# Optimization experiments

Measured on AMD Instinct MI355X. Metric: run time of the kernel, lower is better.

Reference implementation:

```python
import jax, jax.numpy as jnp
import numpy as np

N = 8192   # nodes per graph
F = 128    # input feature dim
H = 512    # GAT hidden dim
D = 256    # GAT output dim (== match_size, required by matching broadcast)
MS = 256   # match_size
E = 131072 # edges per graph (one direction)
EPS = 1e-8 # torch cosine_similarity eps


def _xavier(k, shape):
    lim = (6.0 / (shape[0] + shape[-1])) ** 0.5
    return jax.random.uniform(k, shape, jnp.float32, -lim, lim)


def setup_inputs() -> dict:
    key = jax.random.key(0)
    ks = jax.random.split(key, 24)
    return {
        "x_s": jax.random.normal(ks[0], (N, F), jnp.float32),
        "x_t": jax.random.normal(ks[1], (N, F), jnp.float32),
        "edge_index_s": jax.random.randint(ks[2], (2, E), 0, N),
        "edge_index_t": jax.random.randint(ks[3], (2, E), 0, N),
        "label": jax.random.randint(ks[4], (1,), 0, 2),
        # GAT params (2 single-head layers)
        "W_g1": _xavier(ks[5], (F, H)),
        "a1_src": _xavier(ks[6], (H, 1))[:, 0],
        "a1_dst": _xavier(ks[7], (H, 1))[:, 0],
        "W_g2": _xavier(ks[8], (H, D)),
        "a2_src": _xavier(ks[9], (D, 1))[:, 0],
        "a2_dst": _xavier(ks[10], (D, 1))[:, 0],
        # readout_rep
        "W_read": _xavier(ks[11], (D, D)),
        # matching
        "W_match": _xavier(ks[12], (D, MS)),
        # MLP
        "mlp_w1": _xavier(ks[13], (MS * 8, MS * 2)), "mlp_b1": jnp.zeros((MS * 2,), jnp.float32),
        "mlp_w2": _xavier(ks[14], (MS * 2, MS)),     "mlp_b2": jnp.zeros((MS,), jnp.float32),
        "mlp_w3": _xavier(ks[15], (MS, MS // 2)),    "mlp_b3": jnp.zeros((MS // 2,), jnp.float32),
        "mlp_w4": _xavier(ks[16], (MS // 2, 1)),     "mlp_b4": jnp.zeros((1,), jnp.float32),
    }


def _gat_layer(h_in, src, dst, W, a_s, a_d, n):
    h = h_in @ W                                           # [n, d_out]
    logits = (h[src] * a_s).sum(-1) + (h[dst] * a_d).sum(-1)
    e = jax.nn.leaky_relu(logits, 0.2)
    m = jax.ops.segment_max(e, dst, num_segments=n)
    ex = jnp.exp(e - m[dst])
    den = jax.ops.segment_sum(ex, dst, num_segments=n)
    alpha = ex / (den[dst] + 1e-16)
    return jax.ops.segment_sum(alpha[:, None] * h[src], dst, num_segments=n)


def _gat(x, edge_index, W1, a1s, a1d, W2, a2s, a2d):
    n = x.shape[0]
    sl = jnp.arange(n)
    # symmetrize undirected edge list + add self loops (PyG GATConv convention)
    src = jnp.concatenate([edge_index[0], edge_index[1], sl])
    dst = jnp.concatenate([edge_index[1], edge_index[0], sl])
    h = jax.nn.elu(_gat_layer(x, src, dst, W1, a1s, a1d, n))
    return _gat_layer(h, src, dst, W2, a2s, a2d, n)


def _readout(h, W):
    g = jnp.tanh(jnp.mean(h, 0) @ W)                       # [d]
    s = jax.nn.sigmoid(h @ g)                              # [n]
    return (s[:, None] * h).sum(0, keepdims=True)          # [1, d]


def _match(h1, h2, Wm):
    # cosine over feature dim of (h * W) without materializing [N, D, MS]:
    # dot[n,m] = sum_d h1[n,d]*W[d,m]*h2[n,d]*W[d,m] = ((h1*h2) @ W^2)[n,m]
    W2 = Wm * Wm
    dot = (h1 * h2) @ W2
    n1 = jnp.sqrt((h1 * h1) @ W2)
    n2 = jnp.sqrt((h2 * h2) @ W2)
    return dot / jnp.maximum(n1 * n2, EPS)


def _mutual(h1, h2):
    n1 = jnp.linalg.norm(h1, axis=-1)
    n2 = jnp.linalg.norm(h2, axis=-1)
    cos = (h1 @ h2.T) / jnp.maximum(n1[:, None] * n2[None, :], EPS)  # [N, M]
    coe = cos / cos.sum(0)                                 # column-normalize
    return coe @ h2


def _mlp(z, w1, b1, w2, b2, w3, b3, w4, b4):
    z = jax.nn.relu(z @ w1 + b1)
    z = jax.nn.relu(z @ w2 + b2)
    z = jax.nn.relu(z @ w3 + b3)
    return jax.nn.sigmoid(z @ w4 + b4)


def _forward(x_s, x_t, edge_index_s, edge_index_t, label,
             W_g1, a1_src, a1_dst, W_g2, a2_src, a2_dst,
             W_read, W_match,
             mlp_w1, mlp_b1, mlp_w2, mlp_b2, mlp_w3, mlp_b3, mlp_w4, mlp_b4):
    f1 = (x_s - jnp.mean(x_s)) / jnp.std(x_s, ddof=1)
    f2 = (x_t - jnp.mean(x_t)) / jnp.std(x_t, ddof=1)

    h1 = _gat(f1, edge_index_s, W_g1, a1_src, a1_dst, W_g2, a2_src, a2_dst)
    h2 = _gat(f2, edge_index_t, W_g1, a1_src, a1_dst, W_g2, a2_src, a2_dst)

    h1g = _readout(h1, W_read)
    h2g = _readout(h2, W_read)

    h1m = _mutual(h1, h2)
    h2m = _mutual(h2, h1)
    h1mg = _readout(h1m, W_read)
    h2mg = _readout(h2m, W_read)

    miu1 = _match(h1, h1m, W_match); miu2 = _match(h2, h2m, W_match)
    miu1g = _readout(miu1, W_read);  miu2g = _readout(miu2, W_read)
    phi1 = _match(h1, h1mg, W_match); phi2 = _match(h2, h2mg, W_match)
    phi1g = _readout(phi1, W_read);   phi2g = _readout(phi2, W_read)
    psi1 = _match(h1g, h1m, W_match); psi2 = _match(h2g, h2m, W_match)
    psi1g = _readout(psi1, W_read);   psi2g = _readout(psi2, W_read)
    om1 = _match(h1g, h1mg, W_match); om2 = _match(h2g, h2mg, W_match)

    z1 = jnp.concatenate([miu1g, phi1g, psi1g, om1], axis=1).T  # [4*MS, 1]
    z2 = jnp.concatenate([miu2g, phi2g, psi2g, om2], axis=1).T
    z = jnp.concatenate([z1, z2], axis=0).T                     # [1, 8*MS]
    z = _mlp(z, mlp_w1, mlp_b1, mlp_w2, mlp_b2, mlp_w3, mlp_b3, mlp_w4, mlp_b4)
    return z


def reference(x_s, x_t, edge_index_s, edge_index_t, label,
              W_g1, a1_src, a1_dst, W_g2, a2_src, a2_dst,
              W_read, W_match,
              mlp_w1, mlp_b1, mlp_w2, mlp_b2, mlp_w3, mlp_b3, mlp_w4, mlp_b4):
    z = _forward(x_s, x_t, edge_index_s, edge_index_t, label,
                 W_g1, a1_src, a1_dst, W_g2, a2_src, a2_dst, W_read, W_match,
                 mlp_w1, mlp_b1, mlp_w2, mlp_b2, mlp_w3, mlp_b3, mlp_w4, mlp_b4)
    label_exp = jnp.exp(-label.astype(jnp.float32))
    return z, label, label_exp
```

## Files before the change

kernel.cpp:

```cpp
#include <hip/hip_runtime.h>
#include <hip/hip_bf16.h>
#include <math.h>
#include <stddef.h>

#define NN 8192
#define FF 128
#define HH 512
#define DDIM 256
#define EE 131072
#define ET (2*EE + NN)
#define FEPS 1e-8f

typedef float f32x4 __attribute__((ext_vector_type(4)));
typedef __bf16 bf16x8 __attribute__((ext_vector_type(8)));
typedef unsigned short u16;

static __device__ __forceinline__ u16 f2bf(float f) {
  union { float f; unsigned u; } v; v.f = f;
  return (u16)((v.u + 0x7fffu + ((v.u >> 16) & 1u)) >> 16);
}
static __device__ __forceinline__ float bf2f(u16 h) {
  union { unsigned u; float f; } v; v.u = ((unsigned)h) << 16;
  return v.f;
}
static __device__ __forceinline__ f32x4 mfma16(bf16x8 a, bf16x8 b, f32x4 c) {
  return __builtin_amdgcn_mfma_f32_16x16x32_bf16(a, b, c, 0, 0, 0);
}

struct PLB { const u16* p[6]; int slot[6]; };
struct MM {
  const u16* A1[6]; const u16* A2[6]; const u16* B[6];
  const u16* R1[6]; const u16* R2[6]; const float* Y[6]; u16* o[6];
};

__global__ void k_reduce2(const float* __restrict__ xa, const float* __restrict__ xb,
                          int n, double* __restrict__ out) {
  const float* x = blockIdx.y ? xb : xa;
  double* o = out + 2 * blockIdx.y;
  __shared__ double s1[256], s2[256];
  double a = 0.0, b = 0.0;
  for (int i = blockIdx.x * blockDim.x + threadIdx.x; i < n; i += gridDim.x * blockDim.x) {
    double v = (double)x[i];
    a += v; b += v * v;
  }
  s1[threadIdx.x] = a; s2[threadIdx.x] = b;
  __syncthreads();
  for (int w = 128; w > 0; w >>= 1) {
    if (threadIdx.x < w) { s1[threadIdx.x] += s1[threadIdx.x + w]; s2[threadIdx.x] += s2[threadIdx.x + w]; }
    __syncthreads();
  }
  if (threadIdx.x == 0) { atomicAdd(&o[0], s1[0]); atomicAdd(&o[1], s2[0]); }
}

__global__ void k_normalize2(const float* __restrict__ xa, const float* __restrict__ xb,
                             u16* __restrict__ ya, u16* __restrict__ yb, int n,
                             const double* __restrict__ s) {
  const float* x = blockIdx.y ? xb : xa;
  u16* y = blockIdx.y ? yb : ya;
  const double* sp = s + 2 * blockIdx.y;
  double mean = sp[0] / (double)n;
  double var = (sp[1] - (double)n * mean * mean) / (double)(n - 1);
  float mu = (float)mean;
  float inv = (float)(1.0 / sqrt(var));
  for (int i = blockIdx.x * blockDim.x + threadIdx.x; i < n; i += gridDim.x * blockDim.x)
    y[i] = f2bf((x[i] - mu) * inv);
}

__global__ void k_hist(const int* __restrict__ ei, int* __restrict__ deg) {
  int t = blockIdx.x * blockDim.x + threadIdx.x;
  if (t >= ET) return;
  int dst = (t < EE) ? ei[EE + t] : ((t < 2*EE) ? ei[t - EE] : (t - 2*EE));
  atomicAdd(&deg[dst], 1);
}

__global__ void k_scan(const int* __restrict__ deg, int* __restrict__ offs, int* __restrict__ cursor) {
  __shared__ int ts[256];
  int tid = threadIdx.x;
  int loc[32];
  int s = 0;
  #pragma unroll
  for (int i = 0; i < 32; ++i) { loc[i] = s; s += deg[tid * 32 + i]; }
  ts[tid] = s;
  __syncthreads();
  for (int off = 1; off < 256; off <<= 1) {
    int v = (tid >= off) ? ts[tid - off] : 0;
    __syncthreads();
    ts[tid] += v;
    __syncthreads();
  }
  int pre = ts[tid] - s;
  #pragma unroll
  for (int i = 0; i < 32; ++i) {
    int o = pre + loc[i];
    offs[tid * 32 + i] = o;
    cursor[tid * 32 + i] = o;
  }
  if (tid == 255) offs[NN] = ts[255];
}

__global__ void k_scatter(const int* __restrict__ ei, int* __restrict__ cursor, int* __restrict__ srcs) {
  int t = blockIdx.x * blockDim.x + threadIdx.x;
  if (t >= ET) return;
  int src = (t < 2*EE) ? ei[t] : (t - 2*EE);
  int dst = (t < EE) ? ei[EE + t] : ((t < 2*EE) ? ei[t - EE] : (t - 2*EE));
  int pos = atomicAdd(&cursor[dst], 1);
  srcs[pos] = src;
}

__global__ __launch_bounds__(256) void k_tr_bf16(const float* __restrict__ src, u16* __restrict__ dst,
                                                 int R, int C, int sq) {
  __shared__ float T[32][33];
  int tx = threadIdx.x & 31, ty = threadIdx.x >> 5;
  int r0 = blockIdx.y * 32, c0 = blockIdx.x * 32;
  #pragma unroll
  for (int p = 0; p < 4; ++p)
    T[ty + 8 * p][tx] = src[(size_t)(r0 + ty + 8 * p) * C + c0 + tx];
  __syncthreads();
  #pragma unroll
  for (int p = 0; p < 4; ++p) {
    float v = T[tx][ty + 8 * p];
    if (sq) v *= v;
    dst[(size_t)(c0 + ty + 8 * p) * R + r0 + tx] = f2bf(v);
  }
}

__global__ __launch_bounds__(256) void k_tr2w(const float* __restrict__ hA, const float* __restrict__ scA,
                                              u16* __restrict__ tA, u16* __restrict__ wA,
                                              const float* __restrict__ hB, const float* __restrict__ scB,
                                              u16* __restrict__ tB, u16* __restrict__ wB) {
  __shared__ float T[32][33];
  __shared__ float W[32][33];
  const float* src = blockIdx.z ? hB : hA;
  const float* sc  = blockIdx.z ? scB : scA;
  u16* dt = blockIdx.z ? tB : tA;
  u16* dw = blockIdx.z ? wB : wA;
  int tx = threadIdx.x & 31, ty = threadIdx.x >> 5;
  int r0 = blockIdx.y * 32, c0 = blockIdx.x * 32;
  #pragma unroll
  for (int p = 0; p < 4; ++p) {
    int j = r0 + ty + 8 * p;
    float v = src[(size_t)j * DDIM + c0 + tx];
    T[ty + 8 * p][tx] = v;
    W[ty + 8 * p][tx] = v * sc[j];
  }
  __syncthreads();
  #pragma unroll
  for (int p = 0; p < 4; ++p) {
    size_t o = (size_t)(c0 + ty + 8 * p) * NN + r0 + tx;
    dt[o] = f2bf(T[tx][ty + 8 * p]);
    dw[o] = f2bf(W[tx][ty + 8 * p]);
  }
}

__global__ __launch_bounds__(256) void k_gemm_bf(const u16* __restrict__ A, const u16* __restrict__ Bt,
                                                 u16* __restrict__ Cb, int K, int N,
                                                 const float* __restrict__ as_, const float* __restrict__ ad_,
                                                 float* __restrict__ hs, float* __restrict__ hd) {
  int w = threadIdx.x >> 6, l = threadIdx.x & 63, r15 = l & 15, g = l >> 4;
  int i0 = blockIdx.y * 64 + w * 16;
  int n0 = blockIdx.x * 128;
  f32x4 zero = {0.f, 0.f, 0.f, 0.f};
  f32x4 acc[8];
  #pragma unroll
  for (int n = 0; n < 8; ++n) acc[n] = zero;
  int kcN = K >> 5;
  const u16* arow = A + (size_t)(i0 + r15) * K + g * 8;
  for (int kc = 0; kc < kcN; ++kc) {
    bf16x8 a = *reinterpret_cast<const bf16x8*>(arow + kc * 32);
    #pragma unroll
    for (int n = 0; n < 8; ++n) {
      bf16x8 b = *reinterpret_cast<const bf16x8*>(Bt + (size_t)(n0 + n * 16 + r15) * K + kc * 32 + g * 8);
      acc[n] = mfma16(a, b, acc[n]);
    }
  }
  int io = i0 + g * 4;
  #pragma unroll
  for (int n = 0; n < 8; ++n) {
    int c = n0 + n * 16 + r15;
    #pragma unroll
    for (int q = 0; q < 4; ++q)
      Cb[(size_t)(io + q) * N + c] = f2bf(acc[n][q]);
  }
  if (as_) {
    float hsum[4] = {0.f, 0.f, 0.f, 0.f}, dsum[4] = {0.f, 0.f, 0.f, 0.f};
    #pragma unroll
    for (int n = 0; n < 8; ++n) {
      int c = n0 + n * 16 + r15;
      float av = as_[c], dv = ad_[c];
      #pragma unroll
      for (int q = 0; q < 4; ++q) { hsum[q] += acc[n][q] * av; dsum[q] += acc[n][q] * dv; }
    }
    #pragma unroll
    for (int q = 0; q < 4; ++q) {
      #pragma unroll
      for (int o = 1; o < 16; o <<= 1) { hsum[q] += __shfl_xor(hsum[q], o); dsum[q] += __shfl_xor(dsum[q], o); }
    }
    if (r15 == 0) {
      #pragma unroll
      for (int q = 0; q < 4; ++q) {
        atomicAdd(&hs[io + q], hsum[q]);
        atomicAdd(&hd[io + q], dsum[q]);
      }
    }
  }
}

__global__ void k_alpha(const int* __restrict__ offs, const int* __restrict__ srcs,
                        const float* __restrict__ hs, const float* __restrict__ hd,
                        float* __restrict__ alpha) {
  int wid = (blockIdx.x * blockDim.x + threadIdx.x) >> 6;
  int lane = threadIdx.x & 63;
  if (wid >= NN) return;
  int b = offs[wid], e = offs[wid + 1];
  float hdn = hd[wid];
  float m = -3.4e38f;
  for (int p = b + lane; p < e; p += 64) {
    float v = hs[srcs[p]] + hdn;
    v = v > 0.f ? v : 0.2f * v;
    alpha[p] = v;
    m = fmaxf(m, v);
  }
  #pragma unroll
  for (int o = 32; o > 0; o >>= 1) m = fmaxf(m, __shfl_xor(m, o));
  float den = 0.f;
  for (int p = b + lane; p < e; p += 64) {
    float ex = expf(alpha[p] - m);
    alpha[p] = ex;
    den += ex;
  }
  #pragma unroll
  for (int o = 32; o > 0; o >>= 1) den += __shfl_xor(den, o);
  float sc = 1.f / (den + 1e-16f);
  for (int p = b + lane; p < e; p += 64) alpha[p] *= sc;
}

__global__ __launch_bounds__(256) void k_agg3(const int* __restrict__ offs, const int* __restrict__ srcs,
                                              const float* __restrict__ alpha, const u16* __restrict__ Hb,
                                              float* __restrict__ outF, u16* __restrict__ outB,
                                              int D, int elu) {
  int wv = threadIdx.x >> 6, lane = threadIdx.x & 63;
  int n = blockIdx.x * 4 + wv;
  int b = offs[n], e = offs[n + 1];
  if (D == 512) {
    float acc[8];
    #pragma unroll
    for (int j = 0; j < 8; ++j) acc[j] = 0.f;
    const u16* base = Hb + lane * 8;
    for (int p = b; p < e; ++p) {
      float a = alpha[p];
      uint4 v = *reinterpret_cast<const uint4*>(base + (size_t)srcs[p] * 512);
      acc[0] += a * bf2f((u16)(v.x & 0xffff)); acc[1] += a * bf2f((u16)(v.x >> 16));
      acc[2] += a * bf2f((u16)(v.y & 0xffff)); acc[3] += a * bf2f((u16)(v.y >> 16));
      acc[4] += a * bf2f((u16)(v.z & 0xffff)); acc[5] += a * bf2f((u16)(v.z >> 16));
      acc[6] += a * bf2f((u16)(v.w & 0xffff)); acc[7] += a * bf2f((u16)(v.w >> 16));
    }
    ushort4 o0, o1;
    #pragma unroll
    for (int j = 0; j < 8; ++j)
      if (elu) acc[j] = acc[j] > 0.f ? acc[j] : (expf(acc[j]) - 1.f);
    o0.x = f2bf(acc[0]); o0.y = f2bf(acc[1]); o0.z = f2bf(acc[2]); o0.w = f2bf(acc[3]);
    o1.x = f2bf(acc[4]); o1.y = f2bf(acc[5]); o1.z = f2bf(acc[6]); o1.w = f2bf(acc[7]);
    u16* ob = outB + (size_t)n * 512 + lane * 8;
    *reinterpret_cast<ushort4*>(ob) = o0;
    *reinterpret_cast<ushort4*>(ob + 4) = o1;
  } else {
    float acc[4];
    #pragma unroll
    for (int j = 0; j < 4; ++j) acc[j] = 0.f;
    const u16* base = Hb + lane * 4;
    for (int p = b; p < e; ++p) {
      float a = alpha[p];
      uint2 v = *reinterpret_cast<const uint2*>(base + (size_t)srcs[p] * 256);
      acc[0] += a * bf2f((u16)(v.x & 0xffff)); acc[1] += a * bf2f((u16)(v.x >> 16));
      acc[2] += a * bf2f((u16)(v.y & 0xffff)); acc[3] += a * bf2f((u16)(v.y >> 16));
    }
    #pragma unroll
    for (int j = 0; j < 4; ++j)
      if (elu) acc[j] = acc[j] > 0.f ? acc[j] : (expf(acc[j]) - 1.f);
    if (outF) {
      float4 of = {acc[0], acc[1], acc[2], acc[3]};
      *reinterpret_cast<float4*>(outF + (size_t)n * 256 + lane * 4) = of;
    }
    ushort4 ob;
    ob.x = f2bf(acc[0]); ob.y = f2bf(acc[1]); ob.z = f2bf(acc[2]); ob.w = f2bf(acc[3]);
    *reinterpret_cast<ushort4*>(outB + (size_t)n * 256 + lane * 4) = ob;
  }
}

__global__ void k_rninv2(const float* __restrict__ h1, const float* __restrict__ h2,
                         float* __restrict__ o1, float* __restrict__ o2) {
  const float* h = blockIdx.y ? h2 : h1;
  float* o = blockIdx.y ? o2 : o1;
  int wid = (blockIdx.x * blockDim.x + threadIdx.x) >> 6;
  int lane = threadIdx.x & 63;
  if (wid >= NN) return;
  float4 v = *reinterpret_cast<const float4*>(h + (size_t)wid * DDIM + lane * 4);
  float a = v.x * v.x + v.y * v.y + v.z * v.z + v.w * v.w;
  #pragma unroll
  for (int o2_ = 32; o2_ > 0; o2_ >>= 1) a += __shfl_xor(a, o2_);
  if (!lane) o[wid] = 1.f / sqrtf(a);
}

__global__ void k_wsum(const float* __restrict__ h1, const float* __restrict__ h2,
                       const float* __restrict__ n1inv, const float* __restrict__ n2inv,
                       float* __restrict__ ut) {
  const float* h = blockIdx.y ? h2 : h1;
  const float* wv = blockIdx.y ? n2inv : n1inv;
  float* o = ut + 256 * blockIdx.y;
  int d = threadIdx.x;
  int r0 = blockIdx.x * 128;
  float acc = 0.f;
  for (int r = 0; r < 128; ++r) acc += wv[r0 + r] * h[(size_t)(r0 + r) * 256 + d];
  atomicAdd(&o[d], acc);
}

__global__ void k_rs(const float* __restrict__ h1, const float* __restrict__ h2,
                     const float* __restrict__ n1inv, const float* __restrict__ n2inv,
                     const float* __restrict__ ut, float* __restrict__ R, float* __restrict__ S) {
  const float* h  = blockIdx.y ? h2 : h1;
  const float* ni = blockIdx.y ? n2inv : n1inv;
  const float* gv = blockIdx.y ? ut : ut + 256;
  float* o = blockIdx.y ? S : R;
  int wid = (blockIdx.x * blockDim.x + threadIdx.x) >> 6;
  int lane = threadIdx.x & 63;
  if (wid >= NN) return;
  float4 v = *reinterpret_cast<const float4*>(h + (size_t)wid * 256 + lane * 4);
  float4 g4 = *reinterpret_cast<const float4*>(gv + lane * 4);
  float a = v.x * g4.x + v.y * g4.y + v.z * g4.z + v.w * g4.w;
  #pragma unroll
  for (int o2_ = 32; o2_ > 0; o2_ >>= 1) a += __shfl_xor(a, o2_);
  if (!lane) o[wid] = ni[wid] * a;
}

__global__ void k_scj(const float* __restrict__ S, const float* __restrict__ R,
                      const float* __restrict__ n1inv, const float* __restrict__ n2inv,
                      float* __restrict__ scj1, float* __restrict__ scj2) {
  int j = blockIdx.x * blockDim.x + threadIdx.x;
  if (j >= NN) return;
  scj1[j] = n2inv[j] / S[j];
  scj2[j] = n1inv[j] / R[j];
}

__global__ __launch_bounds__(256) void k_gemm_M(const u16* __restrict__ A1, const u16* __restrict__ B1,
                                                const u16* __restrict__ A2, const u16* __restrict__ B2,
                                                float* __restrict__ Mf) {
  int mat = blockIdx.z & 1, kch = blockIdx.z >> 1;
  const u16* A = mat ? A2 : A1;
  const u16* Bt = mat ? B2 : B1;
  float* C = Mf + mat * 65536;
  int w = threadIdx.x >> 6, l = threadIdx.x & 63, r15 = l & 15, g = l >> 4;
  int i0 = blockIdx.y * 64 + w * 16;
  int n0 = blockIdx.x * 128;
  f32x4 zero = {0.f, 0.f, 0.f, 0.f};
  f32x4 acc[8];
  #pragma unroll
  for (int n = 0; n < 8; ++n) acc[n] = zero;
  const u16* arow = A + (size_t)(i0 + r15) * NN + g * 8;
  for (int kc = kch * 16; kc < kch * 16 + 16; ++kc) {
    bf16x8 a = *reinterpret_cast<const bf16x8*>(arow + kc * 32);
    #pragma unroll
    for (int n = 0; n < 8; ++n) {
      bf16x8 b = *reinterpret_cast<const bf16x8*>(Bt + (size_t)(n0 + n * 16 + r15) * NN + kc * 32 + g * 8);
      acc[n] = mfma16(a, b, acc[n]);
    }
  }
  int io = i0 + g * 4;
  #pragma unroll
  for (int n = 0; n < 8; ++n) {
    int c = n0 + n * 16 + r15;
    #pragma unroll
    for (int q = 0; q < 4; ++q)
      atomicAdd(&C[(size_t)(io + q) * 256 + c], acc[n][q]);
  }
}

__global__ void k_m2bf(const float* __restrict__ Mf, u16* __restrict__ Mb) {
  size_t o = (size_t)blockIdx.y * 65536 + blockIdx.x * 256 + threadIdx.x;
  Mb[o] = f2bf(Mf[o]);
}

__global__ __launch_bounds__(256) void k_gemm_hm(const u16* __restrict__ A1, const u16* __restrict__ M1,
                                                 const float* __restrict__ s1, u16* __restrict__ O1,
                                                 const u16* __restrict__ A2, const u16* __restrict__ M2,
                                                 const float* __restrict__ s2, u16* __restrict__ O2) {
  int z = blockIdx.z;
  const u16* A = z ? A2 : A1;
  const u16* Bt = z ? M2 : M1;
  const float* sc = z ? s2 : s1;
  u16* O = z ? O2 : O1;
  int w = threadIdx.x >> 6, l = threadIdx.x & 63, r15 = l & 15, g = l >> 4;
  int i0 = blockIdx.y * 64 + w * 16;
  int n0 = blockIdx.x * 128;
  f32x4 zero = {0.f, 0.f, 0.f, 0.f};
  f32x4 acc[8];
  #pragma unroll
  for (int n = 0; n < 8; ++n) acc[n] = zero;
  const u16* arow = A + (size_t)(i0 + r15) * 256 + g * 8;
  #pragma unroll
  for (int kc = 0; kc < 8; ++kc) {
    bf16x8 a = *reinterpret_cast<const bf16x8*>(arow + kc * 32);
    #pragma unroll
    for (int n = 0; n < 8; ++n) {
      bf16x8 b = *reinterpret_cast<const bf16x8*>(Bt + (size_t)(n0 + n * 16 + r15) * 256 + kc * 32 + g * 8);
      acc[n] = mfma16(a, b, acc[n]);
    }
  }
  int io = i0 + g * 4;
  float s4[4];
  #pragma unroll
  for (int q = 0; q < 4; ++q) s4[q] = sc[io + q];
  #pragma unroll
  for (int n = 0; n < 8; ++n) {
    int c = n0 + n * 16 + r15;
    #pragma unroll
    for (int q = 0; q < 4; ++q)
      O[(size_t)(io + q) * 256 + c] = f2bf(acc[n][q] * s4[q]);
  }
}

__global__ __launch_bounds__(256) void k_matchA(const u16* __restrict__ A0, const u16* __restrict__ A1,
                                                const u16* __restrict__ A2_, const u16* __restrict__ A3,
                                                const u16* __restrict__ W2t,
                                                u16* __restrict__ r0, u16* __restrict__ r1,
                                                u16* __restrict__ r2, u16* __restrict__ r3) {
  int z = blockIdx.z;
  const u16* A = z == 0 ? A0 : z == 1 ? A1 : z == 2 ? A2_ : A3;
  u16* outR = z == 0 ? r0 : z == 1 ? r1 : z == 2 ? r2 : r3;
  int w = threadIdx.x >> 6, l = threadIdx.x & 63, r15 = l & 15, g = l >> 4;
  int i0 = blockIdx.y * 64 + w * 16;
  int n0 = blockIdx.x * 128;
  f32x4 zero = {0.f, 0.f, 0.f, 0.f};
  f32x4 acc[8];
  #pragma unroll
  for (int n = 0; n < 8; ++n) acc[n] = zero;
  const u16* arow = A + (size_t)(i0 + r15) * 256 + g * 8;
  #pragma unroll
  for (int kc = 0; kc < 8; ++kc) {
    uint4 xv = *reinterpret_cast<const uint4*>(arow + kc * 32);
    bf16x8 fp;
    float t;
    t = bf2f((u16)(xv.x & 0xffff)); fp[0] = (__bf16)(t * t);
    t = bf2f((u16)(xv.x >> 16));    fp[1] = (__bf16)(t * t);
    t = bf2f((u16)(xv.y & 0xffff)); fp[2] = (__bf16)(t * t);
    t = bf2f((u16)(xv.y >> 16));    fp[3] = (__bf16)(t * t);
    t = bf2f((u16)(xv.z & 0xffff)); fp[4] = (__bf16)(t * t);
    t = bf2f((u16)(xv.z >> 16));    fp[5] = (__bf16)(t * t);
    t = bf2f((u16)(xv.w & 0xffff)); fp[6] = (__bf16)(t * t);
    t = bf2f((u16)(xv.w >> 16));    fp[7] = (__bf16)(t * t);
    #pragma unroll
    for (int n = 0; n < 8; ++n) {
      bf16x8 b = *reinterpret_cast<const bf16x8*>(W2t + (size_t)(n0 + n * 16 + r15) * 256 + kc * 32 + g * 8);
      acc[n] = mfma16(fp, b, acc[n]);
    }
  }
  int io = i0 + g * 4;
  #pragma unroll
  for (int n = 0; n < 8; ++n) {
    int c = n0 + n * 16 + r15;
    #pragma unroll
    for (int q = 0; q < 4; ++q)
      outR[(size_t)(io + q) * 256 + c] = f2bf(rsqrtf(fmaxf(acc[n][q], 1e-30f)));
  }
}

__global__ void k_w2d(const u16* __restrict__ W2t, const float* __restrict__ ogs,
                      u16* __restrict__ W2d, float* __restrict__ yn) {
  __shared__ float red[256];
  int n = blockIdx.x, z = blockIdx.y, k = threadIdx.x;
  int map = (z == 0) ? 512 : (z == 1) ? 0 : (z == 2) ? 768 : 256;
  float y = ogs[map + k];
  float wv = bf2f(W2t[n * 256 + k]);
  W2d[z * 65536 + n * 256 + k] = f2bf(wv * y);
  red[k] = wv * y * y;
  __syncthreads();
  for (int s = 128; s > 0; s >>= 1) {
    if (k < s) red[k] += red[k + s];
    __syncthreads();
  }
  if (!k) yn[z * 256 + n] = rsqrtf(fmaxf(red[0], 1e-30f));
}

__global__ __launch_bounds__(256) void k_matchB(MM M) {
  int z = blockIdx.z;
  const u16* A1 = M.A1[z];
  const u16* A2 = M.A2[z];
  const u16* Bt = M.B[z];
  const u16* R1 = M.R1[z];
  const u16* R2 = M.R2[z];
  const float* Y = M.Y[z];
  u16* outb = M.o[z];
  int w = threadIdx.x >> 6, l = threadIdx.x & 63, r15 = l & 15, g = l >> 4;
  int i0 = blockIdx.y * 64 + w * 16;
  int n0 = blockIdx.x * 128;
  f32x4 zero = {0.f, 0.f, 0.f, 0.f};
  f32x4 acc[8];
  #pragma unroll
  for (int n = 0; n < 8; ++n) acc[n] = zero;
  size_t abase = (size_t)(i0 + r15) * 256 + g * 8;
  #pragma unroll
  for (int kc = 0; kc < 8; ++kc) {
    bf16x8 fa;
    uint4 a = *reinterpret_cast<const uint4*>(A1 + abase + kc * 32);
    if (A2) {
      uint4 b2 = *reinterpret_cast<const uint4*>(A2 + abase + kc * 32);
      fa[0] = (__bf16)(bf2f((u16)(a.x & 0xffff)) * bf2f((u16)(b2.x & 0xffff)));
      fa[1] = (__bf16)(bf2f((u16)(a.x >> 16))    * bf2f((u16)(b2.x >> 16)));
      fa[2] = (__bf16)(bf2f((u16)(a.y & 0xffff)) * bf2f((u16)(b2.y & 0xffff)));
      fa[3] = (__bf16)(bf2f((u16)(a.y >> 16))    * bf2f((u16)(b2.y >> 16)));
      fa[4] = (__bf16)(bf2f((u16)(a.z & 0xffff)) * bf2f((u16)(b2.z & 0xffff)));
      fa[5] = (__bf16)(bf2f((u16)(a.z >> 16))    * bf2f((u16)(b2.z >> 16)));
      fa[6] = (__bf16)(bf2f((u16)(a.w & 0xffff)) * bf2f((u16)(b2.w & 0xffff)));
      fa[7] = (__bf16)(bf2f((u16)(a.w >> 16))    * bf2f((u16)(b2.w >> 16)));
    } else {
      fa = *reinterpret_cast<const bf16x8*>(&a);
    }
    #pragma unroll
    for (int n = 0; n < 8; ++n) {
      bf16x8 b = *reinterpret_cast<const bf16x8*>(Bt + (size_t)(n0 + n * 16 + r15) * 256 + kc * 32 + g * 8);
      acc[n] = mfma16(fa, b, acc[n]);
    }
  }
  int io = i0 + g * 4;
  #pragma unroll
  for (int n = 0; n < 8; ++n) {
    int c = n0 + n * 16 + r15;
    float yc = Y ? Y[c] : 1.f;
    #pragma unroll
    for (int q = 0; q < 4; ++q) {
      float sc = yc;
      size_t idx = (size_t)(io + q) * 256 + c;
      if (R1) sc *= bf2f(R1[idx]);
      if (R2) sc *= bf2f(R2[idx]);
      outb[idx] = f2bf(acc[n][q] * sc);
    }
  }
}

__global__ void k_match_g(const float* __restrict__ X1, const float* __restrict__ Y1,
                          const float* __restrict__ X2, const float* __restrict__ Y2,
                          const float* __restrict__ W2, float* __restrict__ v) {
  __shared__ float u[256], p[256], q[256];
  const float* X = blockIdx.x ? X2 : X1;
  const float* Y = blockIdx.x ? Y2 : Y1;
  float* o = v + (blockIdx.x ? 1792 : 768);
  int t = threadIdx.x;
  float xv = X[t], yv = Y[t];
  u[t] = xv * yv; p[t] = xv * xv; q[t] = yv * yv;
  __syncthreads();
  float a = 0.f, b = 0.f, c = 0.f;
  #pragma unroll 4
  for (int d = 0; d < 256; ++d) {
    float wv = W2[(size_t)d * DDIM + t];
    a += u[d] * wv; b += p[d] * wv; c += q[d] * wv;
  }
  o[t] = a / fmaxf(sqrtf(b) * sqrtf(c), FEPS);
}

__global__ void k_w2(const float* __restrict__ Wm, float* __restrict__ W2, int n) {
  int i = blockIdx.x * blockDim.x + threadIdx.x;
  if (i < n) { float v = Wm[i]; W2[i] = v * v; }
}

__global__ void k_bmu_b(PLB L, float* __restrict__ mu) {
  const u16* h = L.p[blockIdx.y];
  int d = threadIdx.x;
  int r0 = blockIdx.x * 128;
  float acc = 0.f;
  for (int r = 0; r < 128; ++r) acc += bf2f(h[(size_t)(r0 + r) * 256 + d]);
  atomicAdd(&mu[blockIdx.y * 256 + d], acc);
}

__global__ void k_bgv(const float* __restrict__ mu, const float* __restrict__ Wr,
                      float* __restrict__ g) {
  __shared__ float ls[256];
  int m = blockIdx.x, t = threadIdx.x;
  ls[t] = mu[m * 256 + t] * (1.f / (float)NN);
  __syncthreads();
  float acc = 0.f;
  #pragma unroll 4
  for (int d = 0; d < 256; ++d) acc += ls[d] * Wr[(size_t)d * 256 + t];
  g[m * 256 + t] = tanhf(acc);
}

__global__ __launch_bounds__(256) void k_bsc_b(PLB L, const float* __restrict__ g,
                                               float* __restrict__ v) {
  __shared__ __align__(16) float gs[256];
  __shared__ float sarr[32];
  int m = blockIdx.y;
  const u16* h = L.p[m];
  int t = threadIdx.x, w = t >> 6, l = t & 63;
  gs[t] = g[m * 256 + t];
  __syncthreads();
  int r0 = blockIdx.x * 32;
  float4 gv4 = reinterpret_cast<const float4*>(gs)[l];
  for (int rr = w * 8; rr < w * 8 + 8; ++rr) {
    ushort4 hv = *reinterpret_cast<const ushort4*>(h + (size_t)(r0 + rr) * 256 + l * 4);
    float dot = bf2f(hv.x) * gv4.x + bf2f(hv.y) * gv4.y + bf2f(hv.z) * gv4.z + bf2f(hv.w) * gv4.w;
    #pragma unroll
    for (int o = 32; o > 0; o >>= 1) dot += __shfl_xor(dot, o);
    if (!l) sarr[rr] = 1.f / (1.f + expf(-dot));
  }
  __syncthreads();
  float acc = 0.f;
  for (int rr = 0; rr < 32; ++rr) acc += sarr[rr] * bf2f(h[(size_t)(r0 + rr) * 256 + t]);
  atomicAdd(&v[L.slot[m] + t], acc);
}

__global__ void k_binit(const float* __restrict__ b1, const float* __restrict__ b2,
                        const float* __restrict__ b3, float* __restrict__ l1,
                        float* __restrict__ l2, float* __restrict__ l3) {
  int t = blockIdx.x * 256 + threadIdx.x;
  if (t < 512) l1[t] = b1[t];
  if (t < 256) l2[t] = b2[t];
  if (t < 128) l3[t] = b3[t];
}

__global__ void k_gemv(const float* __restrict__ vin, const float* __restrict__ w,
                       float* __restrict__ out, int K, int M, int Kc, int relu_in) {
  int m = blockIdx.x * 256 + threadIdx.x;
  if (m >= M) return;
  int k0 = blockIdx.y * Kc;
  float acc = 0.f;
  #pragma unroll 4
  for (int k = k0; k < k0 + Kc; ++k) {
    float x = vin[k];
    if (relu_in) x = fmaxf(x, 0.f);
    acc += x * w[(size_t)k * M + m];
  }
  atomicAdd(&out[m], acc);
}

__global__ void k_final(const float* __restrict__ l3, const float* __restrict__ w4,
                        const float* __restrict__ b4, const int* __restrict__ label,
                        float* __restrict__ out) {
  __shared__ float ls[128];
  int t = threadIdx.x;
  ls[t] = fmaxf(l3[t], 0.f) * w4[t];
  __syncthreads();
  for (int w = 64; w > 0; w >>= 1) { if (t < w) ls[t] += ls[t + w]; __syncthreads(); }
  if (t == 0) {
    float z = 1.f / (1.f + expf(-(ls[0] + b4[0])));
    out[0] = z;
    float lb = (float)label[0];
    out[1] = lb;
    out[2] = expf(-lb);
  }
}

extern "C" void kernel_launch(void* const* d_in, const int* in_sizes, int n_in,
                              void* d_out, int out_size, void* d_ws, size_t ws_size,
                              hipStream_t stream) {
  (void)in_sizes; (void)n_in; (void)out_size;
  const float* x_s   = (const float*)d_in[0];
  const float* x_t   = (const float*)d_in[1];
  const int*   ei_s  = (const int*)d_in[2];
  const int*   ei_t  = (const int*)d_in[3];
  const int*   label = (const int*)d_in[4];
  const float* W_g1  = (const float*)d_in[5];
  const float* a1s   = (const float*)d_in[6];
  const float* a1d   = (const float*)d_in[7];
  const float* W_g2  = (const float*)d_in[8];
  const float* a2s   = (const float*)d_in[9];
  const float* a2d   = (const float*)d_in[10];
  const float* W_read  = (const float*)d_in[11];
  const float* W_match = (const float*)d_in[12];
  const float* w1 = (const float*)d_in[13]; const float* b1 = (const float*)d_in[14];
  const float* w2 = (const float*)d_in[15]; const float* b2 = (const float*)d_in[16];
  const float* w3 = (const float*)d_in[17]; const float* b3 = (const float*)d_in[18];
  const float* w4 = (const float*)d_in[19]; const float* b4 = (const float*)d_in[20];
  float* out = (float*)d_out;

  char* base = (char*)d_ws;
  size_t off = 0;
  auto alloc = [&](size_t bytes) -> void* {
    void* pp = base + off;
    off = (off + bytes + 255) & ~(size_t)255;
    return pp;
  };
  double* dsum = (double*)alloc(4 * sizeof(double));
  u16*   hb_bf= (u16*)alloc((size_t)NN * HH * 2);
  u16*   aggb = (u16*)alloc((size_t)NN * HH * 2);
  float* h1   = (float*)alloc((size_t)NN * DDIM * 4);
  float* h2   = (float*)alloc((size_t)NN * DDIM * 4);
  u16*   f1b  = (u16*)alloc((size_t)NN * FF * 2);
  u16*   f2b  = (u16*)alloc((size_t)NN * FF * 2);
  u16*   h1b  = (u16*)alloc((size_t)NN * DDIM * 2);
  u16*   h2b  = (u16*)alloc((size_t)NN * DDIM * 2);
  u16*   h1mb = (u16*)alloc((size_t)NN * DDIM * 2);
  u16*   h2mb = (u16*)alloc((size_t)NN * DDIM * 2);
  u16*   h1t  = (u16*)alloc((size_t)NN * DDIM * 2);
  u16*   h2t  = (u16*)alloc((size_t)NN * DDIM * 2);
  u16*   wh1t = (u16*)alloc((size_t)NN * DDIM * 2);
  u16*   wh2t = (u16*)alloc((size_t)NN * DDIM * 2);
  u16*   mb0  = (u16*)alloc((size_t)NN * DDIM * 2);
  u16*   mb1  = (u16*)alloc((size_t)NN * DDIM * 2);
  u16*   mb2  = (u16*)alloc((size_t)NN * DDIM * 2);
  u16*   mb3  = (u16*)alloc((size_t)NN * DDIM * 2);
  u16*   mb4  = (u16*)alloc((size_t)NN * DDIM * 2);
  u16*   mb5  = (u16*)alloc((size_t)NN * DDIM * 2);
  u16*   rP1  = (u16*)alloc((size_t)NN * DDIM * 2);
  u16*   rQ1  = (u16*)alloc((size_t)NN * DDIM * 2);
  u16*   rP2  = (u16*)alloc((size_t)NN * DDIM * 2);
  u16*   rQ2  = (u16*)alloc((size_t)NN * DDIM * 2);
  float* alpha= (float*)alloc((size_t)ET * 4);
  int*   srcs = (int*)alloc((size_t)ET * 4);
  int*   deg  = (int*)alloc(NN * 4);
  int*   curs = (int*)alloc(NN * 4);
  int*   offs = (int*)alloc((NN + 1) * 4);
  float* n1inv= (float*)alloc(NN * 4);
  float* n2inv= (float*)alloc(NN * 4);
  float* Rr   = (float*)alloc(NN * 4);
  float* Ss   = (float*)alloc(NN * 4);
  float* scj1 = (float*)alloc(NN * 4);
  float* scj2 = (float*)alloc(NN * 4);
  float* hsb  = (float*)alloc(NN * 4);
  float* hdb  = (float*)alloc(NN * 4);
  float* W2   = (float*)alloc((size_t)DDIM * DDIM * 4);
  u16*   Wg1t = (u16*)alloc((size_t)HH * FF * 2);
  u16*   Wg2t = (u16*)alloc((size_t)DDIM * HH * 2);
  u16*   W2t  = (u16*)alloc((size_t)DDIM * DDIM * 2);
  u16*   W2dB = (u16*)alloc(4 * 65536 * 2);
  float* ynB  = (float*)alloc(4 * 256 * 4);
  u16*   Mb   = (u16*)alloc(2 * 65536 * 2);
  float* mug1 = (float*)alloc(4 * 256 * 4);
  float* ogs  = (float*)alloc(4 * 256 * 4);
  float* mug2 = (float*)alloc(6 * 256 * 4);
  float* v    = (float*)alloc(2048 * 4);
  float* ut   = (float*)alloc(512 * 4);
  float* Mf   = (float*)alloc(2 * 65536 * 4);
  float* g1   = (float*)alloc(4 * 256 * 4);
  float* g2   = (float*)alloc(6 * 256 * 4);
  float* l1o  = (float*)alloc(512 * 4);
  float* l2o  = (float*)alloc(256 * 4);
  float* l3o  = (float*)alloc(128 * 4);
  if (off > ws_size) return;

  float* h1g  = ogs + 0;
  float* h2g  = ogs + 256;
  float* h1mg = ogs + 512;
  float* h2mg = ogs + 768;
  const size_t zr_bytes = (4 * 256 + 4 * 256 + 6 * 256 + 2048 + 512 + 2 * 65536) * 4;

  hipMemsetAsync(dsum, 0, 4 * sizeof(double), stream);
  k_reduce2<<<dim3(1024, 2), 256, 0, stream>>>(x_s, x_t, NN * FF, dsum);
  k_normalize2<<<dim3(1024, 2), 256, 0, stream>>>(x_s, x_t, f1b, f2b, NN * FF, dsum);

  k_tr_bf16<<<dim3(HH / 32, FF / 32), 256, 0, stream>>>(W_g1, Wg1t, FF, HH, 0);
  k_tr_bf16<<<dim3(DDIM / 32, HH / 32), 256, 0, stream>>>(W_g2, Wg2t, HH, DDIM, 0);
  k_tr_bf16<<<dim3(DDIM / 32, DDIM / 32), 256, 0, stream>>>(W_match, W2t, DDIM, DDIM, 1);
  k_w2<<<dim3((DDIM * DDIM + 255) / 256), 256, 0, stream>>>(W_match, W2, DDIM * DDIM);

  auto run_gat = [&](const u16* finb, const int* ei, float* hout, u16* houtb) {
    hipMemsetAsync(deg, 0, NN * 4, stream);
    k_hist<<<dim3((ET + 255) / 256), 256, 0, stream>>>(ei, deg);
    k_scan<<<1, 256, 0, stream>>>(deg, offs, curs);
    k_scatter<<<dim3((ET + 255) / 256), 256, 0, stream>>>(ei, curs, srcs);
    hipMemsetAsync(hsb, 0, 2 * NN * 4, stream);
    k_gemm_bf<<<dim3(HH / 128, NN / 64), 256, 0, stream>>>(finb, Wg1t, hb_bf, FF, HH, a1s, a1d, hsb, hdb);
    k_alpha<<<dim3(NN / 4), 256, 0, stream>>>(offs, srcs, hsb, hdb, alpha);
    k_agg3<<<dim3(NN / 4), 256, 0, stream>>>(offs, srcs, alpha, hb_bf, nullptr, aggb, HH, 1);
    hipMemsetAsync(hsb, 0, 2 * NN * 4, stream);
    k_gemm_bf<<<dim3(DDIM / 128, NN / 64), 256, 0, stream>>>(aggb, Wg2t, hb_bf, HH, DDIM, a2s, a2d, hsb, hdb);
    k_alpha<<<dim3(NN / 4), 256, 0, stream>>>(offs, srcs, hsb, hdb, alpha);
    k_agg3<<<dim3(NN / 4), 256, 0, stream>>>(offs, srcs, alpha, hb_bf, hout, houtb, DDIM, 0);
  };
  run_gat(f1b, ei_s, h1, h1b);
  run_gat(f2b, ei_t, h2, h2b);

  k_rninv2<<<dim3(NN / 4, 2), 256, 0, stream>>>(h1, h2, n1inv, n2inv);
  hipMemsetAsync(mug1, 0, zr_bytes, stream);
  k_wsum<<<dim3(64, 2), 256, 0, stream>>>(h1, h2, n1inv, n2inv, ut);
  k_rs<<<dim3(NN / 4, 2), 256, 0, stream>>>(h1, h2, n1inv, n2inv, ut, Rr, Ss);
  k_scj<<<dim3(NN / 256), 256, 0, stream>>>(Ss, Rr, n1inv, n2inv, scj1, scj2);
  k_tr2w<<<dim3(DDIM / 32, NN / 32, 2), 256, 0, stream>>>(h2, scj1, h2t, wh2t, h1, scj2, h1t, wh1t);
  k_gemm_M<<<dim3(2, 4, 32), 256, 0, stream>>>(wh2t, h2t, wh1t, h1t, Mf);
  k_m2bf<<<dim3(256, 2), 256, 0, stream>>>(Mf, Mb);
  k_gemm_hm<<<dim3(2, 128, 2), 256, 0, stream>>>(h1b, Mb, n1inv, h1mb,
                                                 h2b, Mb + 65536, n2inv, h2mb);

  k_matchA<<<dim3(2, 128, 4), 256, 0, stream>>>(h1b, h1mb, h2b, h2mb, W2t, rP1, rQ1, rP2, rQ2);

  PLB g1l;
  g1l.p[0] = h1b;  g1l.slot[0] = 0;
  g1l.p[1] = h2b;  g1l.slot[1] = 256;
  g1l.p[2] = h1mb; g1l.slot[2] = 512;
  g1l.p[3] = h2mb; g1l.slot[3] = 768;
  k_bmu_b<<<dim3(64, 4), 256, 0, stream>>>(g1l, mug1);
  k_bgv<<<dim3(4), 256, 0, stream>>>(mug1, W_read, g1);
  k_bsc_b<<<dim3(256, 4), 256, 0, stream>>>(g1l, g1, ogs);

  k_w2d<<<dim3(256, 4), 256, 0, stream>>>(W2t, ogs, W2dB, ynB);
  MM m;
  m.A1[0] = h1b;  m.A2[0] = h1mb;    m.B[0] = W2t;            m.R1[0] = rP1; m.R2[0] = rQ1;    m.Y[0] = nullptr;   m.o[0] = mb0;
  m.A1[1] = h1b;  m.A2[1] = nullptr; m.B[1] = W2dB;           m.R1[1] = rP1; m.R2[1] = nullptr; m.Y[1] = ynB;       m.o[1] = mb1;
  m.A1[2] = h1mb; m.A2[2] = nullptr; m.B[2] = W2dB + 65536;   m.R1[2] = rQ1; m.R2[2] = nullptr; m.Y[2] = ynB + 256; m.o[2] = mb2;
  m.A1[3] = h2b;  m.A2[3] = h2mb;    m.B[3] = W2t;            m.R1[3] = rP2; m.R2[3] = rQ2;    m.Y[3] = nullptr;   m.o[3] = mb3;
  m.A1[4] = h2b;  m.A2[4] = nullptr; m.B[4] = W2dB + 2*65536; m.R1[4] = rP2; m.R2[4] = nullptr; m.Y[4] = ynB + 512; m.o[4] = mb4;
  m.A1[5] = h2mb; m.A2[5] = nullptr; m.B[5] = W2dB + 3*65536; m.R1[5] = rQ2; m.R2[5] = nullptr; m.Y[5] = ynB + 768; m.o[5] = mb5;
  k_matchB<<<dim3(2, NN / 64, 6), 256, 0, stream>>>(m);
  k_match_g<<<dim3(2), 256, 0, stream>>>(h1g, h1mg, h2g, h2mg, W2, v);

  PLB g2l;
  g2l.p[0] = mb0; g2l.slot[0] = 0;
  g2l.p[1] = mb1; g2l.slot[1] = 256;
  g2l.p[2] = mb2; g2l.slot[2] = 512;
  g2l.p[3] = mb3; g2l.slot[3] = 1024;
  g2l.p[4] = mb4; g2l.slot[4] = 1280;
  g2l.p[5] = mb5; g2l.slot[5] = 1536;
  k_bmu_b<<<dim3(64, 6), 256, 0, stream>>>(g2l, mug2);
  k_bgv<<<dim3(6), 256, 0, stream>>>(mug2, W_read, g2);
  k_bsc_b<<<dim3(256, 6), 256, 0, stream>>>(g2l, g2, v);

  k_binit<<<dim3(2), 256, 0, stream>>>(b1, b2, b3, l1o, l2o, l3o);
  k_gemv<<<dim3(2, 16), 256, 0, stream>>>(v, w1, l1o, 2048, 512, 128, 0);
  k_gemv<<<dim3(1, 8), 256, 0, stream>>>(l1o, w2, l2o, 512, 256, 64, 1);
  k_gemv<<<dim3(1, 8), 256, 0, stream>>>(l2o, w3, l3o, 256, 128, 32, 1);
  k_final<<<1, 128, 0, stream>>>(l3o, w4, b4, label, out);
}
```

Baseline: 746.4 us.

## Fuse match norm GEMMs and matching GEMMs into one kernel per graph

Merges k_matchA, which computed rsqrt norm matrices and stored them, with k_matchB, which reread them to scale the six matching outputs, into a single kernel. Each block now loads h and hm once and runs five MFMA accumulations (P, Q, U, phi, psi) over a 64-column tile, applying the rsqrt scaling in registers. This removes four NN×256 intermediate buffers, their writes and reads, and one launch. In exchange it holds more accumulator registers per thread, which may lower occupancy.

```diff
diff --git a/kernel.cpp b/kernel.cpp
--- a/kernel.cpp
+++ b/kernel.cpp
@@ -28,10 +28,6 @@
 }
 
 struct PLB { const u16* p[6]; int slot[6]; };
-struct MM {
-  const u16* A1[6]; const u16* A2[6]; const u16* B[6];
-  const u16* R1[6]; const u16* R2[6]; const float* Y[6]; u16* o[6];
-};
 
 __global__ void k_reduce2(const float* __restrict__ xa, const float* __restrict__ xb,
                           int n, double* __restrict__ out) {
@@ -418,51 +414,6 @@
   }
 }
 
-__global__ __launch_bounds__(256) void k_matchA(const u16* __restrict__ A0, const u16* __restrict__ A1,
-                                                const u16* __restrict__ A2_, const u16* __restrict__ A3,
-                                                const u16* __restrict__ W2t,
-                                                u16* __restrict__ r0, u16* __restrict__ r1,
-                                                u16* __restrict__ r2, u16* __restrict__ r3) {
-  int z = blockIdx.z;
-  const u16* A = z == 0 ? A0 : z == 1 ? A1 : z == 2 ? A2_ : A3;
-  u16* outR = z == 0 ? r0 : z == 1 ? r1 : z == 2 ? r2 : r3;
-  int w = threadIdx.x >> 6, l = threadIdx.x & 63, r15 = l & 15, g = l >> 4;
-  int i0 = blockIdx.y * 64 + w * 16;
-  int n0 = blockIdx.x * 128;
-  f32x4 zero = {0.f, 0.f, 0.f, 0.f};
-  f32x4 acc[8];
-  #pragma unroll
-  for (int n = 0; n < 8; ++n) acc[n] = zero;
-  const u16* arow = A + (size_t)(i0 + r15) * 256 + g * 8;
-  #pragma unroll
-  for (int kc = 0; kc < 8; ++kc) {
-    uint4 xv = *reinterpret_cast<const uint4*>(arow + kc * 32);
-    bf16x8 fp;
-    float t;
-    t = bf2f((u16)(xv.x & 0xffff)); fp[0] = (__bf16)(t * t);
-    t = bf2f((u16)(xv.x >> 16));    fp[1] = (__bf16)(t * t);
-    t = bf2f((u16)(xv.y & 0xffff)); fp[2] = (__bf16)(t * t);
-    t = bf2f((u16)(xv.y >> 16));    fp[3] = (__bf16)(t * t);
-    t = bf2f((u16)(xv.z & 0xffff)); fp[4] = (__bf16)(t * t);
-    t = bf2f((u16)(xv.z >> 16));    fp[5] = (__bf16)(t * t);
-    t = bf2f((u16)(xv.w & 0xffff)); fp[6] = (__bf16)(t * t);
-    t = bf2f((u16)(xv.w >> 16));    fp[7] = (__bf16)(t * t);
-    #pragma unroll
-    for (int n = 0; n < 8; ++n) {
-      bf16x8 b = *reinterpret_cast<const bf16x8*>(W2t + (size_t)(n0 + n * 16 + r15) * 256 + kc * 32 + g * 8);
-      acc[n] = mfma16(fp, b, acc[n]);
-    }
-  }
-  int io = i0 + g * 4;
-  #pragma unroll
-  for (int n = 0; n < 8; ++n) {
-    int c = n0 + n * 16 + r15;
-    #pragma unroll
-    for (int q = 0; q < 4; ++q)
-      outR[(size_t)(io + q) * 256 + c] = f2bf(rsqrtf(fmaxf(acc[n][q], 1e-30f)));
-  }
-}
-
 __global__ void k_w2d(const u16* __restrict__ W2t, const float* __restrict__ ogs,
                       u16* __restrict__ W2d, float* __restrict__ yn) {
   __shared__ float red[256];
@@ -480,58 +431,80 @@
   if (!k) yn[z * 256 + n] = rsqrtf(fmaxf(red[0], 1e-30f));
 }
 
-__global__ __launch_bounds__(256) void k_matchB(MM M) {
+__global__ __launch_bounds__(256) void k_match5(
+    const u16* __restrict__ h1b, const u16* __restrict__ h1mb,
+    const u16* __restrict__ h2b, const u16* __restrict__ h2mb,
+    const u16* __restrict__ W2t, const u16* __restrict__ W2dB, const float* __restrict__ ynB,
+    u16* __restrict__ mb0, u16* __restrict__ mb1, u16* __restrict__ mb2,
+    u16* __restrict__ mb3, u16* __restrict__ mb4, u16* __restrict__ mb5) {
   int z = blockIdx.z;
-  const u16* A1 = M.A1[z];
-  const u16* A2 = M.A2[z];
-  const u16* Bt = M.B[z];
-  const u16* R1 = M.R1[z];
-  const u16* R2 = M.R2[z];
-  const float* Y = M.Y[z];
-  u16* outb = M.o[z];
+  const u16* A  = z ? h2b : h1b;
+  const u16* Am = z ? h2mb : h1mb;
+  const u16* Wphi = W2dB + (size_t)(z ? 2 : 0) * 65536;
+  const u16* Wpsi = W2dB + (size_t)(z ? 3 : 1) * 65536;
+  const float* ynphi = ynB + (z ? 512 : 0);
+  const float* ynpsi = ynB + (z ? 768 : 256);
+  u16* oMiu = z ? mb3 : mb0;
+  u16* oPhi = z ? mb4 : mb1;
+  u16* oPsi = z ? mb5 : mb2;
   int w = threadIdx.x >> 6, l = threadIdx.x & 63, r15 = l & 15, g = l >> 4;
   int i0 = blockIdx.y * 64 + w * 16;
-  int n0 = blockIdx.x * 128;
+  int n0 = blockIdx.x * 64;
   f32x4 zero = {0.f, 0.f, 0.f, 0.f};
-  f32x4 acc[8];
-  #pragma unroll
-  for (int n = 0; n < 8; ++n) acc[n] = zero;
+  f32x4 aP[4], aQ[4], aU[4], aD1[4], aD2[4];
+  #pragma unroll
+  for (int n = 0; n < 4; ++n) { aP[n] = zero; aQ[n] = zero; aU[n] = zero; aD1[n] = zero; aD2[n] = zero; }
   size_t abase = (size_t)(i0 + r15) * 256 + g * 8;
-  #pragma unroll
+  #pragma unroll 2
   for (int kc = 0; kc < 8; ++kc) {
-    bf16x8 fa;
-    uint4 a = *reinterpret_cast<const uint4*>(A1 + abase + kc * 32);
-    if (A2) {
-      uint4 b2 = *reinterpret_cast<const uint4*>(A2 + abase + kc * 32);
-      fa[0] = (__bf16)(bf2f((u16)(a.x & 0xffff)) * bf2f((u16)(b2.x & 0xffff)));
-      fa[1] = (__bf16)(bf2f((u16)(a.x >> 16))    * bf2f((u16)(b2.x >> 16)));
-      fa[2] = (__bf16)(bf2f((u16)(a.y & 0xffff)) * bf2f((u16)(b2.y & 0xffff)));
-      fa[3] = (__bf16)(bf2f((u16)(a.y >> 16))    * bf2f((u16)(b2.y >> 16)));
-      fa[4] = (__bf16)(bf2f((u16)(a.z & 0xffff)) * bf2f((u16)(b2.z & 0xffff)));
-      fa[5] = (__bf16)(bf2f((u16)(a.z >> 16))    * bf2f((u16)(b2.z >> 16)));
-      fa[6] = (__bf16)(bf2f((u16)(a.w & 0xffff)) * bf2f((u16)(b2.w & 0xffff)));
-      fa[7] = (__bf16)(bf2f((u16)(a.w >> 16))    * bf2f((u16)(b2.w >> 16)));
-    } else {
-      fa = *reinterpret_cast<const bf16x8*>(&a);
-    }
-    #pragma unroll
-    for (int n = 0; n < 8; ++n) {
-      bf16x8 b = *reinterpret_cast<const bf16x8*>(Bt + (size_t)(n0 + n * 16 + r15) * 256 + kc * 32 + g * 8);
-      acc[n] = mfma16(fa, b, acc[n]);
+    uint4 xa = *reinterpret_cast<const uint4*>(A + abase + kc * 32);
+    uint4 xc = *reinterpret_cast<const uint4*>(Am + abase + kc * 32);
+    bf16x8 fa = *reinterpret_cast<const bf16x8*>(&xa);
+    bf16x8 fc = *reinterpret_cast<const bf16x8*>(&xc);
+    bf16x8 fu, fp, fq;
+    float ta, tc;
+    ta = bf2f((u16)(xa.x & 0xffff)); tc = bf2f((u16)(xc.x & 0xffff));
+    fu[0] = (__bf16)(ta * tc); fp[0] = (__bf16)(ta * ta); fq[0] = (__bf16)(tc * tc);
+    ta = bf2f((u16)(xa.x >> 16));    tc = bf2f((u16)(xc.x >> 16));
+    fu[1] = (__bf16)(ta * tc); fp[1] = (__bf16)(ta * ta); fq[1] = (__bf16)(tc * tc);
+    ta = bf2f((u16)(xa.y & 0xffff)); tc = bf2f((u16)(xc.y & 0xffff));
+    fu[2] = (__bf16)(ta * tc); fp[2] = (__bf16)(ta * ta); fq[2] = (__bf16)(tc * tc);
+    ta = bf2f((u16)(xa.y >> 16));    tc = bf2f((u16)(xc.y >> 16));
+    fu[3] = (__bf16)(ta * tc); fp[3] = (__bf16)(ta * ta); fq[3] = (__bf16)(tc * tc);
+    ta = bf2f((u16)(xa.z & 0xffff)); tc = bf2f((u16)(xc.z & 0xffff));
+    fu[4] = (__bf16)(ta * tc); fp[4] = (__bf16)(ta * ta); fq[4] = (__bf16)(tc * tc);
+    ta = bf2f((u16)(xa.z >> 16));    tc = bf2f((u16)(xc.z >> 16));
+    fu[5] = (__bf16)(ta * tc); fp[5] = (__bf16)(ta * ta); fq[5] = (__bf16)(tc * tc);
+    ta = bf2f((u16)(xa.w & 0xffff)); tc = bf2f((u16)(xc.w & 0xffff));
+    fu[6] = (__bf16)(ta * tc); fp[6] = (__bf16)(ta * ta); fq[6] = (__bf16)(tc * tc);
+    ta = bf2f((u16)(xa.w >> 16));    tc = bf2f((u16)(xc.w >> 16));
+    fu[7] = (__bf16)(ta * tc); fp[7] = (__bf16)(ta * ta); fq[7] = (__bf16)(tc * tc);
+    #pragma unroll
+    for (int n = 0; n < 4; ++n) {
+      size_t boff = (size_t)(n0 + n * 16 + r15) * 256 + kc * 32 + g * 8;
+      bf16x8 bw = *reinterpret_cast<const bf16x8*>(W2t + boff);
+      aP[n] = mfma16(fp, bw, aP[n]);
+      aQ[n] = mfma16(fq, bw, aQ[n]);
+      aU[n] = mfma16(fu, bw, aU[n]);
+      bf16x8 b1 = *reinterpret_cast<const bf16x8*>(Wphi + boff);
+      aD1[n] = mfma16(fa, b1, aD1[n]);
+      bf16x8 b2 = *reinterpret_cast<const bf16x8*>(Wpsi + boff);
+      aD2[n] = mfma16(fc, b2, aD2[n]);
     }
   }
   int io = i0 + g * 4;
   #pragma unroll
-  for (int n = 0; n < 8; ++n) {
+  for (int n = 0; n < 4; ++n) {
     int c = n0 + n * 16 + r15;
-    float yc = Y ? Y[c] : 1.f;
+    float y1 = ynphi[c], y2 = ynpsi[c];
     #pragma unroll
     for (int q = 0; q < 4; ++q) {
-      float sc = yc;
+      float rp = rsqrtf(fmaxf(aP[n][q], 1e-30f));
+      float rq = rsqrtf(fmaxf(aQ[n][q], 1e-30f));
       size_t idx = (size_t)(io + q) * 256 + c;
-      if (R1) sc *= bf2f(R1[idx]);
-      if (R2) sc *= bf2f(R2[idx]);
-      outb[idx] = f2bf(acc[n][q] * sc);
+      oMiu[idx] = f2bf(aU[n][q] * rp * rq);
+      oPhi[idx] = f2bf(aD1[n][q] * rp * y1);
+      oPsi[idx] = f2bf(aD2[n][q] * rq * y2);
     }
   }
 }
@@ -698,10 +671,6 @@
   u16*   mb3  = (u16*)alloc((size_t)NN * DDIM * 2);
   u16*   mb4  = (u16*)alloc((size_t)NN * DDIM * 2);
   u16*   mb5  = (u16*)alloc((size_t)NN * DDIM * 2);
-  u16*   rP1  = (u16*)alloc((size_t)NN * DDIM * 2);
-  u16*   rQ1  = (u16*)alloc((size_t)NN * DDIM * 2);
-  u16*   rP2  = (u16*)alloc((size_t)NN * DDIM * 2);
-  u16*   rQ2  = (u16*)alloc((size_t)NN * DDIM * 2);
   float* alpha= (float*)alloc((size_t)ET * 4);
   int*   srcs = (int*)alloc((size_t)ET * 4);
   int*   deg  = (int*)alloc(NN * 4);
@@ -778,8 +747,6 @@
   k_gemm_hm<<<dim3(2, 128, 2), 256, 0, stream>>>(h1b, Mb, n1inv, h1mb,
                                                  h2b, Mb + 65536, n2inv, h2mb);
 
-  k_matchA<<<dim3(2, 128, 4), 256, 0, stream>>>(h1b, h1mb, h2b, h2mb, W2t, rP1, rQ1, rP2, rQ2);
-
   PLB g1l;
   g1l.p[0] = h1b;  g1l.slot[0] = 0;
   g1l.p[1] = h2b;  g1l.slot[1] = 256;
@@ -790,14 +757,8 @@
   k_bsc_b<<<dim3(256, 4), 256, 0, stream>>>(g1l, g1, ogs);
 
   k_w2d<<<dim3(256, 4), 256, 0, stream>>>(W2t, ogs, W2dB, ynB);
-  MM m;
-  m.A1[0] = h1b;  m.A2[0] = h1mb;    m.B[0] = W2t;            m.R1[0] = rP1; m.R2[0] = rQ1;    m.Y[0] = nullptr;   m.o[0] = mb0;
-  m.A1[1] = h1b;  m.A2[1] = nullptr; m.B[1] = W2dB;           m.R1[1] = rP1; m.R2[1] = nullptr; m.Y[1] = ynB;       m.o[1] = mb1;
-  m.A1[2] = h1mb; m.A2[2] = nullptr; m.B[2] = W2dB + 65536;   m.R1[2] = rQ1; m.R2[2] = nullptr; m.Y[2] = ynB + 256; m.o[2] = mb2;
-  m.A1[3] = h2b;  m.A2[3] = h2mb;    m.B[3] = W2t;            m.R1[3] = rP2; m.R2[3] = rQ2;    m.Y[3] = nullptr;   m.o[3] = mb3;
-  m.A1[4] = h2b;  m.A2[4] = nullptr; m.B[4] = W2dB + 2*65536; m.R1[4] = rP2; m.R2[4] = nullptr; m.Y[4] = ynB + 512; m.o[4] = mb4;
-  m.A1[5] = h2mb; m.A2[5] = nullptr; m.B[5] = W2dB + 3*65536; m.R1[5] = rQ2; m.R2[5] = nullptr; m.Y[5] = ynB + 768; m.o[5] = mb5;
-  k_matchB<<<dim3(2, NN / 64, 6), 256, 0, stream>>>(m);
+  k_match5<<<dim3(4, 128, 2), 256, 0, stream>>>(h1b, h1mb, h2b, h2mb, W2t, W2dB, ynB,
+                                                mb0, mb1, mb2, mb3, mb4, mb5);
   k_match_g<<<dim3(2), 256, 0, stream>>>(h1g, h1mg, h2g, h2mg, W2, v);
 
   PLB g2l;
```

New measurement: 696.9 us. 6.6% less time.
